# Performance work log

Measured on AMD Instinct MI355X. Metric: run time of the kernel, lower is better.

## Reference

```python
import jax, jax.numpy as jnp
import numpy as np

N, E, F_NODE, F_EDGE, H, EH, G = 20000, 200000, 32, 8, 256, 16, 512
OUT_DIMS = [H, H, H // 2]  # 256, 256, 128
BN_EPS = 1e-5


def _lin(k, out_c, in_c):
    kw, kb = jax.random.split(k)
    bound = 1.0 / np.sqrt(in_c)
    w = jax.random.uniform(kw, (out_c, in_c), minval=-bound, maxval=bound, dtype=jnp.float32)
    b = jax.random.uniform(kb, (out_c,), minval=-bound, maxval=bound, dtype=jnp.float32)
    return w, b


def setup_inputs() -> dict:
    key = jax.random.key(0)
    ks = jax.random.split(key, 40)
    inp = {
        "x": jax.random.normal(ks[0], (N, F_NODE), dtype=jnp.float32),
        "edge_index": jax.random.randint(ks[1], (2, E), 0, N, dtype=jnp.int64),
        "edge_attr": jax.random.normal(ks[2], (E, F_EDGE), dtype=jnp.float32),
        "batch": jnp.sort(jax.random.randint(ks[3], (N,), 0, G, dtype=jnp.int64)),
    }
    inp["ee_w"], inp["ee_b"] = _lin(ks[4], EH, F_EDGE)
    inp["ne_w"], inp["ne_b"] = _lin(ks[5], H, F_NODE)
    in_dim = H
    for i, out_dim in enumerate(OUT_DIMS):
        msg_in = 2 * in_dim + EH
        inp[f"c{i}_w1"], inp[f"c{i}_b1"] = _lin(ks[6 + 2 * i], 2 * out_dim, msg_in)
        inp[f"c{i}_w2"], inp[f"c{i}_b2"] = _lin(ks[7 + 2 * i], out_dim, 2 * out_dim)
        inp[f"bn{i}_g"] = jnp.ones((out_dim,), jnp.float32)
        inp[f"bn{i}_b"] = jnp.zeros((out_dim,), jnp.float32)
        inp[f"bn{i}_m"] = jnp.zeros((out_dim,), jnp.float32)
        inp[f"bn{i}_v"] = jnp.ones((out_dim,), jnp.float32)
        in_dim = out_dim
    inp["fc_w"], inp["fc_b"] = _lin(ks[20], 12, H // 2)
    return inp


def _seg_mean(vals, idx, num):
    s = jax.ops.segment_sum(vals, idx, num_segments=num)
    cnt = jax.ops.segment_sum(jnp.ones((vals.shape[0],), vals.dtype), idx, num_segments=num)
    return s / jnp.maximum(cnt, 1.0)[:, None]


def reference(x, edge_index, edge_attr, batch,
              ee_w, ee_b, ne_w, ne_b,
              c0_w1, c0_b1, c0_w2, c0_b2,
              c1_w1, c1_b1, c1_w2, c1_b2,
              c2_w1, c2_b1, c2_w2, c2_b2,
              bn0_g, bn0_b, bn0_m, bn0_v,
              bn1_g, bn1_b, bn1_m, bn1_v,
              bn2_g, bn2_b, bn2_m, bn2_v,
              fc_w, fc_b):
    src, dst = edge_index[0], edge_index[1]  # x_j = source, x_i = target
    e = jax.nn.relu(edge_attr @ ee_w.T + ee_b)  # [E, EH]
    h = jax.nn.relu(x @ ne_w.T + ne_b)          # [N, H]
    convs = [(c0_w1, c0_b1, c0_w2, c0_b2), (c1_w1, c1_b1, c1_w2, c1_b2), (c2_w1, c2_b1, c2_w2, c2_b2)]
    bns = [(bn0_g, bn0_b, bn0_m, bn0_v), (bn1_g, bn1_b, bn1_m, bn1_v), (bn2_g, bn2_b, bn2_m, bn2_v)]
    for (w1, b1, w2, b2), (g, bb, rm, rv) in zip(convs, bns):
        m = jnp.concatenate([h[dst], h[src], e], axis=1)      # [E, 2*in + EH]
        m = jax.nn.relu(m @ w1.T + b1) @ w2.T + b2            # per-edge MLP
        h = _seg_mean(m, dst, N)                              # scatter-mean to targets
        h = jax.nn.relu((h - rm) / jnp.sqrt(rv + BN_EPS) * g + bb)  # eval-mode BN
        # dropout is identity in eval mode
    pooled = _seg_mean(h, batch, G)                           # global_mean_pool [G, H//2]
    return jax.nn.sigmoid(pooled @ fc_w.T + fc_b)             # [G, 12]
```

## Files before the change

### kernel.cpp

```cpp
#include <hip/hip_runtime.h>
#include <hip/hip_bf16.h>

typedef unsigned int  uint;
typedef unsigned short ushort;
typedef float  f32x2  __attribute__((ext_vector_type(2)));
typedef float  f32x4  __attribute__((ext_vector_type(4)));
typedef __bf16 bf16x8 __attribute__((ext_vector_type(8)));

#define DEV static __device__ __forceinline__

DEV float  b2f(ushort b){ return __uint_as_float(((uint)b) << 16); }
DEV float  lo2f(uint u){ return __uint_as_float(u << 16); }
DEV float  hi2f(uint u){ return __uint_as_float(u & 0xffff0000u); }
DEV ushort f2b(float f){
  uint u = __float_as_uint(f);
  u += 0x7fffu + ((u >> 16) & 1u);
  return (ushort)(u >> 16);
}
DEV uint pk2(float a, float b){ return (uint)f2b(a) | ((uint)f2b(b) << 16); }
DEV void unpack8(uint4 v, float* f){
  f[0]=lo2f(v.x); f[1]=hi2f(v.x); f[2]=lo2f(v.y); f[3]=hi2f(v.y);
  f[4]=lo2f(v.z); f[5]=hi2f(v.z); f[6]=lo2f(v.w); f[7]=hi2f(v.w);
}
DEV int ld_idx(const void* p, int flag, long long i){
  return flag ? ((const int*)p)[i] : (int)((const long long*)p)[i];
}
DEV float ldf(const void* p, int f, int i){
  return f ? ((const float*)p)[i] : b2f(((const ushort*)p)[i]);
}
DEV int clampi(int v, int lo, int hi){ return v < lo ? lo : (v > hi ? hi : v); }

DEV void ld16(const ushort* g, ushort* l){
  __builtin_amdgcn_global_load_lds(
      (const __attribute__((address_space(1))) void*)g,
      (__attribute__((address_space(3))) void*)l, 16, 0, 0);
}

__global__ __launch_bounds__(256) void k_zero_probe(const uint* __restrict__ ei,
    const uint* __restrict__ xw, int* __restrict__ iflag, int* __restrict__ fflag,
    int* __restrict__ zbase, int zn){
  int i = blockIdx.x*256 + threadIdx.x;
  if (i < zn) zbase[i] = 0;
  if (blockIdx.x == 0){
    __shared__ int anyI, cntF;
    if (threadIdx.x == 0){ anyI = 0; cntF = 0; }
    __syncthreads();
    int li = 0, lc = 0;
    for (int k = threadIdx.x; k < 1024; k += 256){
      if (ei[2*k + 1] != 0u) li = 1;
      float f = fabsf(__uint_as_float(xw[k]));
      if (f > 1e-6f && f < 1e6f) lc++;
    }
    if (li) atomicOr(&anyI, 1);
    atomicAdd(&cntF, lc);
    __syncthreads();
    if (threadIdx.x == 0){ *iflag = anyI; *fflag = (2*cntF > 1024) ? 1 : 0; }
  }
}

__global__ __launch_bounds__(256) void k_count(const void* __restrict__ ei,
    const int* __restrict__ flag, int* __restrict__ cnt, int E, int N){
  int e = blockIdx.x*256 + threadIdx.x;
  if (e >= E) return;
  int d = clampi(ld_idx(ei, *flag, (long long)E + e), 0, N-1);
  atomicAdd(&cnt[d], 1);
}

__global__ __launch_bounds__(1024) void k_scan(const int* __restrict__ deg, int* __restrict__ rp, int n){
  __shared__ int part[1024];
  int t = threadIdx.x;
  int chunk = (n + 1023) >> 10;
  int base = t * chunk;
  int s = 0;
  for (int i = 0; i < chunk; i++){ int j = base + i; if (j < n) s += deg[j]; }
  part[t] = s;
  __syncthreads();
  for (int off = 1; off < 1024; off <<= 1){
    int v = (t >= off) ? part[t - off] : 0;
    __syncthreads();
    part[t] += v;
    __syncthreads();
  }
  int run = part[t] - s;
  for (int i = 0; i < chunk; i++){ int j = base + i; if (j < n){ rp[j] = run; run += deg[j]; } }
  if (t == 1023) rp[n] = part[1023];
}

struct CvtTab { const void* src[6]; ushort* dst[6]; int n[6]; int bstart[6]; int nseg; };

__global__ __launch_bounds__(256) void k_mega(
    const void* __restrict__ ei, const int* __restrict__ iflag,
    const int* __restrict__ rp, int* __restrict__ fill, int2* __restrict__ cpair,
    CvtTab ct, const int* __restrict__ fflag,
    const void* __restrict__ ea, const void* __restrict__ eew, const void* __restrict__ eeb,
    const void* __restrict__ x, const void* __restrict__ nw, const void* __restrict__ nbias,
    float* __restrict__ eh, ushort* __restrict__ h,
    int E, int N, int FB, int CB, int EB){
  int b = blockIdx.x;
  int t = threadIdx.x;
  if (b < FB){
    int e = b*256 + t;
    if (e >= E) return;
    int f = *iflag;
    int s = clampi(ld_idx(ei, f, e), 0, N-1);
    int d = clampi(ld_idx(ei, f, (long long)E + e), 0, N-1);
    int pos = clampi(rp[d] + atomicAdd(&fill[d], 1), 0, E-1);
    cpair[pos] = make_int2(s, e);
  } else if (b < FB + CB){
    int cb = b - FB;
    int s = ct.nseg - 1;
    for (int i = 1; i < ct.nseg; i++) if (cb < ct.bstart[i]){ s = i - 1; break; }
    int rel = cb - ct.bstart[s];
    const void* sp = ct.src[s];
    ushort* d = ct.dst[s];
    int f = *fflag;
    int end = ct.n[s]; int cap = rel*8192 + 8192; if (cap < end) end = cap;
    for (int i = rel*8192 + t; i < end; i += 256)
      d[i] = f ? f2b(((const float*)sp)[i]) : ((const ushort*)sp)[i];
  } else if (b < FB + CB + EB){
    __shared__ float ws[128];
    __shared__ float bs[16];
    int f = *fflag;
    if (t < 128) ws[t] = ldf(eew, f, t);
    if (t < 16)  bs[t] = ldf(eeb, f, t);
    __syncthreads();
    int e = (b - FB - CB)*256 + t;
    if (e >= E) return;
    float a[8];
    if (f){
      const float4* ap = (const float4*)((const float*)ea + (size_t)e*8);
      float4 v0 = ap[0], v1 = ap[1];
      a[0]=v0.x; a[1]=v0.y; a[2]=v0.z; a[3]=v0.w;
      a[4]=v1.x; a[5]=v1.y; a[6]=v1.z; a[7]=v1.w;
    } else {
      uint4 av = *(const uint4*)((const ushort*)ea + (size_t)e*8);
      unpack8(av, a);
    }
    float o[16];
    #pragma unroll
    for (int c = 0; c < 16; c++){
      float s = bs[c];
      #pragma unroll
      for (int j = 0; j < 8; j++) s += a[j]*ws[c*8+j];
      o[c] = fmaxf(s, 0.f);
    }
    f32x4* op = (f32x4*)(eh + (size_t)e*16);
    #pragma unroll
    for (int q4 = 0; q4 < 4; q4++){
      f32x4 v = {o[q4*4+0], o[q4*4+1], o[q4*4+2], o[q4*4+3]};
      op[q4] = v;
    }
  } else {
    __shared__ float xs[4][32];
    int f = *fflag;
    int nb = (b - FB - CB - EB)*4;
    if (t < 128){
      int ni = t >> 5, ci = t & 31;
      int n = nb + ni; if (n >= N) n = N - 1;
      xs[ni][ci] = f ? ((const float*)x)[(size_t)n*32 + ci]
                     : b2f(((const ushort*)x)[(size_t)n*32 + ci]);
    }
    __syncthreads();
    float wr[32];
    if (f){
      const float4* wp = (const float4*)((const float*)nw + (size_t)t*32);
      #pragma unroll
      for (int q4 = 0; q4 < 8; q4++){
        float4 v = wp[q4];
        wr[q4*4+0]=v.x; wr[q4*4+1]=v.y; wr[q4*4+2]=v.z; wr[q4*4+3]=v.w;
      }
    } else {
      const uint4* wp = (const uint4*)((const ushort*)nw + (size_t)t*32);
      unpack8(wp[0], wr); unpack8(wp[1], wr+8); unpack8(wp[2], wr+16); unpack8(wp[3], wr+24);
    }
    float bv = ldf(nbias, f, t);
    #pragma unroll
    for (int ni = 0; ni < 4; ni++){
      int n = nb + ni;
      if (n >= N) break;
      float s = bv;
      #pragma unroll
      for (int k = 0; k < 32; k++) s += xs[ni][k]*wr[k];
      h[(size_t)n*256 + t] = f2b(fmaxf(s, 0.f));
    }
  }
}

__global__ __launch_bounds__(256) void k_gemm_pq_lds(const ushort* __restrict__ A,
    const ushort* __restrict__ w1, int M, int Nc,
    ushort* __restrict__ P, ushort* __restrict__ Q){
  __shared__ ushort As[128*32];
  __shared__ ushort Bs[128*32];
  const int t = threadIdx.x;
  const int lane = t & 63;
  const int wv = t >> 6;
  const int m0 = blockIdx.x*128;
  const int yc = Nc >> 7;
  const int isQ = (int)blockIdx.y >= yc;
  const int n0 = (isQ ? blockIdx.y - yc : blockIdx.y)*128;
  const ushort* W = w1 + (isQ ? 256 : 0);
  ushort* C = isQ ? Q : P;
  const int lr = lane & 15;
  const int qq = lane >> 4;
  int srow0 = t >> 2,         sq0 = t & 3;
  int srow1 = (256 + t) >> 2, sq1 = t & 3;
  int ga0 = m0 + srow0; if (ga0 >= M) ga0 = M - 1;
  int ga1 = m0 + srow1; if (ga1 >= M) ga1 = M - 1;
  f32x4 acc[2][8];
  #pragma unroll
  for (int f = 0; f < 2; f++)
    #pragma unroll
    for (int j = 0; j < 8; j++) acc[f][j] = {0.f,0.f,0.f,0.f};
  for (int k0 = 0; k0 < 256; k0 += 32){
    ld16(A + (size_t)ga0*256 + k0 + sq0*8, &As[(size_t)t*8]);
    ld16(A + (size_t)ga1*256 + k0 + sq1*8, &As[(size_t)(256+t)*8]);
    ld16(W + (size_t)(n0 + srow0)*528 + k0 + sq0*8, &Bs[(size_t)t*8]);
    ld16(W + (size_t)(n0 + srow1)*528 + k0 + sq1*8, &Bs[(size_t)(256+t)*8]);
    __syncthreads();
    bf16x8 a0 = *(const bf16x8*)&As[(wv*32 + lr)*32 + qq*8];
    bf16x8 a1 = *(const bf16x8*)&As[(wv*32 + 16 + lr)*32 + qq*8];
    #pragma unroll
    for (int j = 0; j < 8; j++){
      bf16x8 b = *(const bf16x8*)&Bs[(j*16 + lr)*32 + qq*8];
      acc[0][j] = __builtin_amdgcn_mfma_f32_16x16x32_bf16(a0, b, acc[0][j], 0, 0, 0);
      acc[1][j] = __builtin_amdgcn_mfma_f32_16x16x32_bf16(a1, b, acc[1][j], 0, 0, 0);
    }
    __syncthreads();
  }
  #pragma unroll
  for (int f = 0; f < 2; f++){
    #pragma unroll
    for (int r = 0; r < 4; r++){
      int row = m0 + wv*32 + f*16 + qq*4 + r;
      if (row >= M) continue;
      #pragma unroll
      for (int j = 0; j < 8; j++)
        C[(size_t)row*Nc + n0 + j*16 + lr] = f2b(acc[f][j][r]);
    }
  }
}

__global__ __launch_bounds__(256) void k_gemm_bn64(const ushort* __restrict__ A, int lda,
    const ushort* __restrict__ W, int ldb, int M, int Nc, int K,
    const void* __restrict__ bias, const void* __restrict__ g, const void* __restrict__ bb,
    const void* __restrict__ rm, const void* __restrict__ rv, const int* __restrict__ fflag,
    const int* __restrict__ rp, ushort* __restrict__ H){
  __shared__ ushort As[64*32];
  __shared__ ushort Bs[128*32];
  const int t = threadIdx.x;
  const int lane = t & 63;
  const int wv = t >> 6;
  const int m0 = blockIdx.x*64;
  const int n0 = blockIdx.y*128;
  const int lr = lane & 15;
  const int qq = lane >> 4;
  int srowA = t >> 2, sqA = t & 3;
  int ga = m0 + srowA; if (ga >= M) ga = M - 1;
  int srowB0 = t >> 2,        srowB1 = 64 + (t >> 2);
  f32x4 acc[8];
  #pragma unroll
  for (int j = 0; j < 8; j++) acc[j] = {0.f,0.f,0.f,0.f};
  for (int k0 = 0; k0 < K; k0 += 32){
    ld16(A + (size_t)ga*lda + k0 + sqA*8, &As[(size_t)t*8]);
    ld16(W + (size_t)(n0 + srowB0)*ldb + k0 + sqA*8, &Bs[(size_t)t*8]);
    ld16(W + (size_t)(n0 + srowB1)*ldb + k0 + sqA*8, &Bs[(size_t)(256+t)*8]);
    __syncthreads();
    bf16x8 a = *(const bf16x8*)&As[(wv*16 + lr)*32 + qq*8];
    #pragma unroll
    for (int j = 0; j < 8; j++){
      bf16x8 b = *(const bf16x8*)&Bs[(j*16 + lr)*32 + qq*8];
      acc[j] = __builtin_amdgcn_mfma_f32_16x16x32_bf16(a, b, acc[j], 0, 0, 0);
    }
    __syncthreads();
  }
  int f = *fflag;
  float bi[8], sc[8], sh[8];
  #pragma unroll
  for (int j = 0; j < 8; j++){
    int col = n0 + j*16 + lr;
    bi[j] = ldf(bias, f, col);
    sc[j] = ldf(g, f, col) * rsqrtf(ldf(rv, f, col) + 1e-5f);
    sh[j] = ldf(bb, f, col) - ldf(rm, f, col) * sc[j];
  }
  #pragma unroll
  for (int r = 0; r < 4; r++){
    int row = m0 + wv*16 + qq*4 + r;
    if (row >= M) continue;
    int empty = (rp[row+1] - rp[row] == 0);
    #pragma unroll
    for (int j = 0; j < 8; j++){
      float v = acc[j][r] + bi[j];
      if (empty) v = 0.f;
      H[(size_t)row*Nc + n0 + j*16 + lr] = f2b(fmaxf(v*sc[j] + sh[j], 0.f));
    }
  }
}

template<int C>
__global__ __launch_bounds__(256) void k_msg4(const ushort* P, const ushort* __restrict__ Q,
    const float* __restrict__ eh, const ushort* __restrict__ w1, const void* __restrict__ b1,
    const int* __restrict__ fflag, const int* __restrict__ rp, const int2* __restrict__ cpair,
    ushort* MU, int N){
  int t = threadIdx.x;
  int c0 = t*2;
  f32x2 wc[16];
  {
    float a0[16], a1[16];
    const uint4* wp0 = (const uint4*)(w1 + (size_t)c0*528 + 512);
    const uint4* wp1 = (const uint4*)(w1 + (size_t)(c0+1)*528 + 512);
    unpack8(wp0[0], a0); unpack8(wp0[1], a0+8);
    unpack8(wp1[0], a1); unpack8(wp1[1], a1+8);
    #pragma unroll
    for (int j = 0; j < 16; j++){ wc[j].x = a0[j]; wc[j].y = a1[j]; }
  }
  int ff = *fflag;
  f32x2 b1v = { ldf(b1, ff, c0), ldf(b1, ff, c0+1) };
  int nb = blockIdx.x*2;
  int ne = nb + 2; if (ne > N) ne = N;
  for (int n = nb; n < ne; n++){
    const int i0 = rp[n], i1 = rp[n+1];
    uint pw = *(const uint*)(P + (size_t)n*C + c0);
    f32x2 pre = { lo2f(pw) + b1v.x, hi2f(pw) + b1v.y };
    f32x2 acc0 = {0.f, 0.f}, acc1 = {0.f, 0.f};
    int i = i0;
    int2 p0, p1; uint qw0, qw1;
    if (i + 2 <= i1){
      p0 = cpair[i]; p1 = cpair[i+1];
      qw0 = *(const uint*)(Q + (size_t)p0.x*C + c0);
      qw1 = *(const uint*)(Q + (size_t)p1.x*C + c0);
    }
    while (i + 2 <= i1){
      int inx = i + 2;
      bool more = (inx + 2 <= i1);
      int2 np0, np1;
      if (more){ np0 = cpair[inx]; np1 = cpair[inx+1]; }
      const f32x4* e0p = (const f32x4*)(eh + (size_t)p0.y*16);
      const f32x4* e1p = (const f32x4*)(eh + (size_t)p1.y*16);
      f32x4 ea0 = e0p[0], ea1 = e0p[1], ea2 = e0p[2], ea3 = e0p[3];
      f32x4 eb0 = e1p[0], eb1 = e1p[1], eb2 = e1p[2], eb3 = e1p[3];
      uint nq0 = 0, nq1 = 0;
      if (more){
        nq0 = *(const uint*)(Q + (size_t)np0.x*C + c0);
        nq1 = *(const uint*)(Q + (size_t)np1.x*C + c0);
      }
      float ef0[16] = {ea0.x,ea0.y,ea0.z,ea0.w, ea1.x,ea1.y,ea1.z,ea1.w,
                       ea2.x,ea2.y,ea2.z,ea2.w, ea3.x,ea3.y,ea3.z,ea3.w};
      float ef1[16] = {eb0.x,eb0.y,eb0.z,eb0.w, eb1.x,eb1.y,eb1.z,eb1.w,
                       eb2.x,eb2.y,eb2.z,eb2.w, eb3.x,eb3.y,eb3.z,eb3.w};
      f32x2 d0 = { pre.x + lo2f(qw0), pre.y + hi2f(qw0) };
      f32x2 d1 = { pre.x + lo2f(qw1), pre.y + hi2f(qw1) };
      #pragma unroll
      for (int j = 0; j < 16; j++){
        f32x2 e0v = {ef0[j], ef0[j]};
        f32x2 e1v = {ef1[j], ef1[j]};
        d0 += wc[j] * e0v;
        d1 += wc[j] * e1v;
      }
      acc0.x += fmaxf(d0.x, 0.f); acc0.y += fmaxf(d0.y, 0.f);
      acc1.x += fmaxf(d1.x, 0.f); acc1.y += fmaxf(d1.y, 0.f);
      if (more){ p0 = np0; p1 = np1; qw0 = nq0; qw1 = nq1; }
      i = inx;
    }
    if (i < i1){
      int2 t0 = cpair[i];
      uint tq0 = *(const uint*)(Q + (size_t)t0.x*C + c0);
      const f32x4* e0p = (const f32x4*)(eh + (size_t)t0.y*16);
      f32x4 ea0 = e0p[0], ea1 = e0p[1], ea2 = e0p[2], ea3 = e0p[3];
      float ef0[16] = {ea0.x,ea0.y,ea0.z,ea0.w, ea1.x,ea1.y,ea1.z,ea1.w,
                       ea2.x,ea2.y,ea2.z,ea2.w, ea3.x,ea3.y,ea3.z,ea3.w};
      f32x2 d0 = { pre.x + lo2f(tq0), pre.y + hi2f(tq0) };
      #pragma unroll
      for (int j = 0; j < 16; j++){
        f32x2 e0v = {ef0[j], ef0[j]};
        d0 += wc[j] * e0v;
      }
      acc0.x += fmaxf(d0.x, 0.f); acc0.y += fmaxf(d0.y, 0.f);
    }
    int cnt = i1 - i0;
    float inv = (cnt > 0) ? 1.f/(float)cnt : 0.f;
    *(uint*)(MU + (size_t)n*C + c0) = pk2((acc0.x + acc1.x)*inv, (acc0.y + acc1.y)*inv);
  }
}

__global__ __launch_bounds__(128) void k_pool(const ushort* __restrict__ h, const void* __restrict__ batch,
    const int* __restrict__ iflag, const void* __restrict__ fw, const void* __restrict__ fb,
    const int* __restrict__ fflag, void* __restrict__ out, int N){
  int g = blockIdx.x, t = threadIdx.x;
  int ifl = *iflag;
  int lo = 0, hi = N;
  while (lo < hi){ int mid = (lo+hi) >> 1; if (ld_idx(batch, ifl, mid) <  g) lo = mid+1; else hi = mid; }
  int s0 = lo;
  hi = N;
  while (lo < hi){ int mid = (lo+hi) >> 1; if (ld_idx(batch, ifl, mid) <= g) lo = mid+1; else hi = mid; }
  int s1 = lo;
  float s = 0.f;
  for (int i = s0; i < s1; i++) s += b2f(h[(size_t)i*128 + t]);
  int cnt = s1 - s0;
  __shared__ float ps[128];
  ps[t] = s / (float)(cnt > 0 ? cnt : 1);
  __syncthreads();
  int f = *fflag;
  if (t < 12){
    float z = ldf(fb, f, t);
    for (int j = 0; j < 128; j++) z += ps[j]*ldf(fw, f, t*128 + j);
    float r = 1.f/(1.f + expf(-z));
    if (f) ((float*)out)[g*12 + t] = r;
    else   ((ushort*)out)[g*12 + t] = f2b(r);
  }
}

__global__ __launch_bounds__(256) void k_sentinel(ushort* __restrict__ out, int n){
  int i = blockIdx.x*256 + threadIdx.x;
  if (i < n) out[i] = 0x3F00;
}

extern "C" void kernel_launch(void* const* d_in, const int* in_sizes, int n_in,
                              void* d_out, int out_size, void* d_ws, size_t ws_size,
                              hipStream_t stream){
  const void* x_raw   = d_in[0];
  const void* ei_raw  = d_in[1];
  const void* ea_raw  = d_in[2];
  const void* ba_raw  = d_in[3];
  (void)n_in;

  const int N = in_sizes[3];
  const int E = in_sizes[1] / 2;
  const int G = out_size / 12;

  char* base = (char*)d_ws;
  size_t off = 0;
  auto alloc = [&](size_t bytes)->char*{
    char* p = base + off;
    off = (off + bytes + 255) & ~(size_t)255;
    return p;
  };
  int* iflag    = (int*)alloc(256);
  int* fflag    = (int*)alloc(256);
  int* deg      = (int*)alloc((size_t)N*4);
  int* fill     = (int*)alloc((size_t)N*4);
  int zn        = (int)(fill - deg) + N;
  int* rp       = (int*)alloc((size_t)(N+1)*4);
  int2* cpair   = (int2*)alloc((size_t)E*8);
  ushort* w1c[3], *w2c[3];
  const int w1n[3] = {512*528, 512*528, 256*528};
  const int w2n[3] = {256*512, 256*512, 128*256};
  for (int i = 0; i < 3; i++) w1c[i] = (ushort*)alloc((size_t)w1n[i]*2);
  for (int i = 0; i < 3; i++) w2c[i] = (ushort*)alloc((size_t)w2n[i]*2);
  float*  e_h32 = (float*)alloc((size_t)E*16*4);
  ushort* h     = (ushort*)alloc((size_t)N*256*2);
  ushort* Q     = (ushort*)alloc((size_t)N*512*2);
  ushort* PM    = (ushort*)alloc((size_t)N*512*2);

  if (off > ws_size){
    k_sentinel<<<(out_size + 255)/256, 256, 0, stream>>>((ushort*)d_out, out_size);
    return;
  }

  k_zero_probe<<<(zn + 255)/256, 256, 0, stream>>>((const uint*)ei_raw, (const uint*)x_raw,
                                                   iflag, fflag, deg, zn);
  k_count<<<(E + 255)/256, 256, 0, stream>>>(ei_raw, iflag, deg, E, N);
  k_scan<<<1, 1024, 0, stream>>>(deg, rp, N);

  CvtTab ct; ct.nseg = 6;
  const void* csrcs[6] = {d_in[8], d_in[16], d_in[24], d_in[10], d_in[18], d_in[26]};
  ushort* cdsts[6]     = {w1c[0],  w1c[1],   w1c[2],   w2c[0],   w2c[1],   w2c[2]};
  const int cns[6]     = {w1n[0],  w1n[1],   w1n[2],   w2n[0],   w2n[1],   w2n[2]};
  int bacc = 0;
  for (int i = 0; i < 6; i++){
    ct.src[i] = csrcs[i]; ct.dst[i] = cdsts[i]; ct.n[i] = cns[i];
    ct.bstart[i] = bacc; bacc += (cns[i] + 8191)/8192;
  }
  int FB = (E + 255)/256;
  int CB = bacc;
  int EB = (E + 255)/256;
  int NB = (N + 3)/4;
  k_mega<<<FB + CB + EB + NB, 256, 0, stream>>>(
      ei_raw, iflag, rp, fill, cpair, ct, fflag,
      ea_raw, d_in[4], d_in[5], x_raw, d_in[6], d_in[7],
      e_h32, h, E, N, FB, CB, EB);

  const int Cch[3] = {512, 512, 256};
  const int Od[3]  = {256, 256, 128};
  for (int i = 0; i < 3; i++){
    int di = 8 + 8*i;
    dim3 g1((N + 127)/128, 2*(Cch[i]/128));
    k_gemm_pq_lds<<<g1, 256, 0, stream>>>(h, w1c[i], N, Cch[i], PM, Q);
    dim3 gm((N + 1)/2);
    if (i < 2) k_msg4<512><<<gm, 256, 0, stream>>>(PM, Q, e_h32, w1c[i], d_in[di+1], fflag, rp, cpair, PM, N);
    else       k_msg4<256><<<gm, 128, 0, stream>>>(PM, Q, e_h32, w1c[i], d_in[di+1], fflag, rp, cpair, PM, N);
    dim3 g2((N + 63)/64, Od[i]/128 > 0 ? Od[i]/128 : 1);
    k_gemm_bn64<<<g2, 256, 0, stream>>>(PM, Cch[i], w2c[i], Cch[i], N, Od[i], Cch[i],
                                        d_in[di+3], d_in[di+4], d_in[di+5],
                                        d_in[di+6], d_in[di+7], fflag, rp, h);
  }

  k_pool<<<G, 128, 0, stream>>>(h, ba_raw, iflag, d_in[32], d_in[33], fflag, d_out, N);
}
```

Before: 501.8 us.

## Reorder edge features into CSR order and swizzle GEMM block mapping

```diff
diff --git a/kernel.cpp b/kernel.cpp
--- a/kernel.cpp
+++ b/kernel.cpp
@@ -186,18 +186,34 @@
   }
 }
 
+__global__ __launch_bounds__(256) void k_reorder(const int2* __restrict__ cpair,
+    const float* __restrict__ eh, float* __restrict__ ehp, int E){
+  int c = blockIdx.x*256 + threadIdx.x;
+  if (c >= E*4) return;
+  int pos = c >> 2, q = c & 3;
+  int e = cpair[pos].y;
+  ((f32x4*)ehp)[(size_t)pos*4 + q] = ((const f32x4*)eh)[(size_t)e*4 + q];
+}
+
 __global__ __launch_bounds__(256) void k_gemm_pq_lds(const ushort* __restrict__ A,
     const ushort* __restrict__ w1, int M, int Nc,
     ushort* __restrict__ P, ushort* __restrict__ Q){
+  const int MT = (M + 127) >> 7;
+  const int YC = Nc >> 6;
+  int jb = blockIdx.x;
+  int gx = jb & 7, rr = jb >> 3;
+  int sx = rr / YC, yy = rr % YC;
+  const int Tm = sx*8 + gx;
+  if (Tm >= MT) return;
   __shared__ ushort As[128*32];
   __shared__ ushort Bs[128*32];
   const int t = threadIdx.x;
   const int lane = t & 63;
   const int wv = t >> 6;
-  const int m0 = blockIdx.x*128;
+  const int m0 = Tm*128;
   const int yc = Nc >> 7;
-  const int isQ = (int)blockIdx.y >= yc;
-  const int n0 = (isQ ? blockIdx.y - yc : blockIdx.y)*128;
+  const int isQ = yy >= yc;
+  const int n0 = (isQ ? yy - yc : yy)*128;
   const ushort* W = w1 + (isQ ? 256 : 0);
   ushort* C = isQ ? Q : P;
   const int lr = lane & 15;
@@ -245,13 +261,20 @@
     const void* __restrict__ bias, const void* __restrict__ g, const void* __restrict__ bb,
     const void* __restrict__ rm, const void* __restrict__ rv, const int* __restrict__ fflag,
     const int* __restrict__ rp, ushort* __restrict__ H){
+  const int MT = (M + 63) >> 6;
+  const int YC = Nc >> 7;
+  int jb = blockIdx.x;
+  int gx = jb & 7, rr = jb >> 3;
+  int sx = rr / YC, yy = rr % YC;
+  const int Tm = sx*8 + gx;
+  if (Tm >= MT) return;
   __shared__ ushort As[64*32];
   __shared__ ushort Bs[128*32];
   const int t = threadIdx.x;
   const int lane = t & 63;
   const int wv = t >> 6;
-  const int m0 = blockIdx.x*64;
-  const int n0 = blockIdx.y*128;
+  const int m0 = Tm*64;
+  const int n0 = yy*128;
   const int lr = lane & 15;
   const int qq = lane >> 4;
   int srowA = t >> 2, sqA = t & 3;
@@ -298,7 +321,7 @@
 
 template<int C>
 __global__ __launch_bounds__(256) void k_msg4(const ushort* P, const ushort* __restrict__ Q,
-    const float* __restrict__ eh, const ushort* __restrict__ w1, const void* __restrict__ b1,
+    const float* __restrict__ ehp, const ushort* __restrict__ w1, const void* __restrict__ b1,
     const int* __restrict__ fflag, const int* __restrict__ rp, const int2* __restrict__ cpair,
     ushort* MU, int N){
   int t = threadIdx.x;
@@ -334,8 +357,8 @@
       bool more = (inx + 2 <= i1);
       int2 np0, np1;
       if (more){ np0 = cpair[inx]; np1 = cpair[inx+1]; }
-      const f32x4* e0p = (const f32x4*)(eh + (size_t)p0.y*16);
-      const f32x4* e1p = (const f32x4*)(eh + (size_t)p1.y*16);
+      const f32x4* e0p = (const f32x4*)(ehp + (size_t)i*16);
+      const f32x4* e1p = (const f32x4*)(ehp + (size_t)(i+1)*16);
       f32x4 ea0 = e0p[0], ea1 = e0p[1], ea2 = e0p[2], ea3 = e0p[3];
       f32x4 eb0 = e1p[0], eb1 = e1p[1], eb2 = e1p[2], eb3 = e1p[3];
       uint nq0 = 0, nq1 = 0;
@@ -364,7 +387,7 @@
     if (i < i1){
       int2 t0 = cpair[i];
       uint tq0 = *(const uint*)(Q + (size_t)t0.x*C + c0);
-      const f32x4* e0p = (const f32x4*)(eh + (size_t)t0.y*16);
+      const f32x4* e0p = (const f32x4*)(ehp + (size_t)i*16);
       f32x4 ea0 = e0p[0], ea1 = e0p[1], ea2 = e0p[2], ea3 = e0p[3];
       float ef0[16] = {ea0.x,ea0.y,ea0.z,ea0.w, ea1.x,ea1.y,ea1.z,ea1.w,
                        ea2.x,ea2.y,ea2.z,ea2.w, ea3.x,ea3.y,ea3.z,ea3.w};
@@ -447,6 +470,7 @@
   for (int i = 0; i < 3; i++) w1c[i] = (ushort*)alloc((size_t)w1n[i]*2);
   for (int i = 0; i < 3; i++) w2c[i] = (ushort*)alloc((size_t)w2n[i]*2);
   float*  e_h32 = (float*)alloc((size_t)E*16*4);
+  float*  ehp32 = (float*)alloc((size_t)E*16*4);
   ushort* h     = (ushort*)alloc((size_t)N*256*2);
   ushort* Q     = (ushort*)alloc((size_t)N*512*2);
   ushort* PM    = (ushort*)alloc((size_t)N*512*2);
@@ -479,16 +503,20 @@
       ea_raw, d_in[4], d_in[5], x_raw, d_in[6], d_in[7],
       e_h32, h, E, N, FB, CB, EB);
 
+  k_reorder<<<(E*4 + 255)/256, 256, 0, stream>>>(cpair, e_h32, ehp32, E);
+
   const int Cch[3] = {512, 512, 256};
   const int Od[3]  = {256, 256, 128};
+  const int MTpq = (N + 127)/128;
+  const int MTbn = (N + 63)/64;
   for (int i = 0; i < 3; i++){
     int di = 8 + 8*i;
-    dim3 g1((N + 127)/128, 2*(Cch[i]/128));
+    int g1 = 8 * ((MTpq + 7)/8) * (Cch[i] >> 6);
     k_gemm_pq_lds<<<g1, 256, 0, stream>>>(h, w1c[i], N, Cch[i], PM, Q);
     dim3 gm((N + 1)/2);
-    if (i < 2) k_msg4<512><<<gm, 256, 0, stream>>>(PM, Q, e_h32, w1c[i], d_in[di+1], fflag, rp, cpair, PM, N);
-    else       k_msg4<256><<<gm, 128, 0, stream>>>(PM, Q, e_h32, w1c[i], d_in[di+1], fflag, rp, cpair, PM, N);
-    dim3 g2((N + 63)/64, Od[i]/128 > 0 ? Od[i]/128 : 1);
+    if (i < 2) k_msg4<512><<<gm, 256, 0, stream>>>(PM, Q, ehp32, w1c[i], d_in[di+1], fflag, rp, cpair, PM, N);
+    else       k_msg4<256><<<gm, 128, 0, stream>>>(PM, Q, ehp32, w1c[i], d_in[di+1], fflag, rp, cpair, PM, N);
+    int g2 = 8 * ((MTbn + 7)/8) * (Od[i] >> 7);
     k_gemm_bn64<<<g2, 256, 0, stream>>>(PM, Cch[i], w2c[i], Cch[i], N, Od[i], Cch[i],
                                         d_in[di+3], d_in[di+4], d_in[di+5],
                                         d_in[di+6], d_in[di+7], fflag, rp, h);
```

Measured after the change: 486.0 us. 1.03x faster.
